# Optimization experiments

Measured on AMD Instinct MI355X. Metric: run time of the kernel, lower is better.

## Reference

```python
import jax, jax.numpy as jnp
import numpy as np

B, C, O, H, W, K, KS = 32, 128, 128, 56, 56, 4, 3
EPS = 1e-5


def setup_inputs() -> dict:
    key = jax.random.key(0)
    ks = jax.random.split(key, 6)
    sc = lambda k, shape, s: jax.random.normal(k, shape, jnp.float32) * s
    return {
        "x": jax.random.normal(ks[0], (B, C, H, W), jnp.float32),
        "fc1_w": sc(ks[1], (K, C), 0.05),
        "fc1_b": jnp.zeros((K,), jnp.float32),
        "fc2_w": sc(ks[2], (K, K), 0.3),
        "fc2_b": jnp.zeros((K,), jnp.float32),
        "weight": sc(ks[3], (K, O, C, KS, KS), 0.05),  # [K, out, in/groups, kh, kw]
        "bias": sc(ks[4], (K, O), 0.05),
        "gamma": jnp.ones((O,), jnp.float32),
        "beta": jnp.zeros((O,), jnp.float32),
    }


def reference(x, fc1_w, fc1_b, fc2_w, fc2_b, weight, bias, gamma, beta):
    # attention2d: global avg pool -> 1x1 conv (== linear) -> relu -> 1x1 conv -> softmax over K
    pooled = x.mean(axis=(2, 3))                          # [B, C]
    h = jax.nn.relu(pooled @ fc1_w.T + fc1_b)             # [B, K]
    attn = jax.nn.softmax(h @ fc2_w.T + fc2_b, axis=-1)   # [B, K]

    # per-sample aggregated kernel / bias
    agg_w = jnp.einsum('bk,koihw->boihw', attn, weight)   # [B, O, C, KS, KS]
    agg_b = attn @ bias                                    # [B, O]

    # per-sample conv (== groups=batch trick in torch)
    def conv_one(xi, wi):
        return jax.lax.conv_general_dilated(
            xi[None], wi, window_strides=(1, 1),
            padding=((1, 1), (1, 1)),
            dimension_numbers=('NCHW', 'OIHW', 'NCHW'))[0]

    out = jax.vmap(conv_one)(x, agg_w) + agg_b[:, :, None, None]  # [B, O, H, W]

    # BatchNorm2d in training mode: biased batch stats over (N, H, W)
    mean = out.mean(axis=(0, 2, 3))
    var = out.var(axis=(0, 2, 3))
    out = (out - mean[None, :, None, None]) * jax.lax.rsqrt(var + EPS)[None, :, None, None]
    out = out * gamma[None, :, None, None] + beta[None, :, None, None]
    return jax.nn.relu(out)
```

## Files before the change

kernel.cpp:

```cpp
#include <hip/hip_runtime.h>
#include <hip/hip_bf16.h>

#define BB 32
#define CC 128
#define OO 128
#define HH 56
#define WW 56
#define KK 4
#define HW 3136
#define WPLANE 147456
#define EPSV 1e-5f

#define NP4 232
#define BUF4 15360

typedef __attribute__((ext_vector_type(8))) short short8v;
typedef __attribute__((ext_vector_type(4))) float f32x4;

static __device__ __forceinline__ void gload16(const void* g, void* l) {
    __builtin_amdgcn_global_load_lds((const __attribute__((address_space(1))) void*)g,
                                     (__attribute__((address_space(3))) void*)l, 16, 0, 0);
}

__global__ void convert_pool_kernel(const float* __restrict__ x,
                                    ushort* __restrict__ xbf,
                                    float* __restrict__ pooledp,
                                    ushort* __restrict__ zpage) {
    const int h = blockIdx.x, b = blockIdx.y;
    if (h == 0 && b == 0 && threadIdx.x < 32) zpage[threadIdx.x] = 0;
    __shared__ float4 xl4[1792];
    const float* xp = x + (size_t)(b * CC) * HW + h * WW;

    #pragma unroll
    for (int k = 0; k < 7; ++k) {
        int u = threadIdx.x + k * 256;
        int c = u / 14, w4 = u - c * 14;
        float4 v = *(const float4*)(xp + (size_t)c * HW + w4 * 4);
        xl4[u ^ ((c >> 3) & 7)] = v;
    }
    __syncthreads();

    const float* xf = (const float*)xl4;
    #pragma unroll
    for (int k = 0; k < 4; ++k) {
        int v = threadIdx.x + k * 256;
        if (v < 896) {
            int w = v >> 4, c8 = v & 15;
            int w4 = w >> 2, wo = w & 3;
            short8v res;
            #pragma unroll
            for (int j = 0; j < 8; ++j) {
                int c = c8 * 8 + j;
                int su = (c * 14 + w4) ^ (c8 & 7);
                __hip_bfloat16 hb = __float2bfloat16(xf[su * 4 + wo]);
                res[j] = *(short*)&hb;
            }
            *(short8v*)(xbf + ((size_t)((b * HH + h) * WW + w)) * CC + c8 * 8) = res;
        }
    }

    if (threadIdx.x < 128) {
        int c = threadIdx.x;
        float s = 0.f;
        #pragma unroll
        for (int w4 = 0; w4 < 14; ++w4) {
            float4 v = xl4[(c * 14 + w4) ^ ((c >> 3) & 7)];
            s += v.x + v.y + v.z + v.w;
        }
        pooledp[((size_t)(b * HH + h)) * CC + c] = s;
    }
}

__global__ void attn_kernel(const float* __restrict__ pooledp,
                            const float* __restrict__ fc1_w, const float* __restrict__ fc1_b,
                            const float* __restrict__ fc2_w, const float* __restrict__ fc2_b,
                            float* __restrict__ attn) {
    const int b = blockIdx.x, c = threadIdx.x;
    float s = 0.f;
    for (int h = 0; h < HH; ++h) s += pooledp[((size_t)(b * HH + h)) * CC + c];
    const float pc = s * (1.0f / HW);
    __shared__ float red[8];
    const int lane = c & 63, wid = c >> 6;
    #pragma unroll
    for (int k = 0; k < KK; ++k) {
        float v = pc * fc1_w[k * CC + c];
        for (int off = 32; off > 0; off >>= 1) v += __shfl_down(v, off, 64);
        if (lane == 0) red[k * 2 + wid] = v;
    }
    __syncthreads();
    if (c == 0) {
        float hk[KK], z[KK], m = -1e30f, den = 0.f;
        #pragma unroll
        for (int k = 0; k < KK; ++k)
            hk[k] = fmaxf(red[k * 2] + red[k * 2 + 1] + fc1_b[k], 0.f);
        #pragma unroll
        for (int k = 0; k < KK; ++k) {
            float t = fc2_b[k];
            #pragma unroll
            for (int j = 0; j < KK; ++j) t += hk[j] * fc2_w[k * KK + j];
            z[k] = t; m = fmaxf(m, t);
        }
        #pragma unroll
        for (int k = 0; k < KK; ++k) { z[k] = expf(z[k] - m); den += z[k]; }
        #pragma unroll
        for (int k = 0; k < KK; ++k) attn[b * KK + k] = z[k] / den;
    }
}

__global__ void aggw_kernel(const float* __restrict__ attn, const float* __restrict__ weight,
                            const float* __restrict__ bias,
                            ushort* __restrict__ aggw, float* __restrict__ agg_b) {
    int idx = blockIdx.x * 256 + threadIdx.x;
    if (idx < BB * 9 * OO * CC) {
        int cc = idx & 31;
        int t1 = idx >> 5;
        int o  = t1 & 127;
        int t2 = t1 >> 7;
        int ci = t2 & 3;
        int t3 = t2 >> 2;
        int j  = t3 % 9;
        int b  = t3 / 9;
        int c  = ci * 32 + cc;
        size_t wi = ((size_t)(o * CC + c)) * 9 + j;
        float s = attn[b*KK + 0] * weight[wi]
                + attn[b*KK + 1] * weight[wi + (size_t)WPLANE]
                + attn[b*KK + 2] * weight[wi + (size_t)2*WPLANE]
                + attn[b*KK + 3] * weight[wi + (size_t)3*WPLANE];
        __hip_bfloat16 hb = __float2bfloat16(s);
        aggw[idx] = *(ushort*)&hb;
    }
    if (blockIdx.x < 16) {
        int i = blockIdx.x * 256 + threadIdx.x;
        int b = i >> 7, o = i & 127;
        float s = 0.f;
        #pragma unroll
        for (int k = 0; k < KK; ++k) s += attn[b*KK + k] * bias[k*OO + o];
        agg_b[i] = s;
    }
}

__launch_bounds__(256, 2)
__global__ void conv_kernel(const ushort* __restrict__ xbf, const ushort* __restrict__ aggw,
                            const float* __restrict__ agg_b, const ushort* __restrict__ zpage,
                            float* __restrict__ out,
                            float* __restrict__ psum, float* __restrict__ psumsq) {
    const int lid  = blockIdx.x;
    const int gwid = (lid & 7) * 112 + (lid >> 3);
    const int b = gwid / 28;
    const int t = gwid - b * 28;
    const int h0 = t * 2;
    __shared__ ushort xs[2 * BUF4 / 2];

    const int tid  = threadIdx.x;
    const int lane = tid & 63;
    const int wid  = tid >> 6;
    const int cf = lane & 15;
    const int kg = lane >> 4;

    const ushort* gp[4]; int gstep[4];
    #pragma unroll
    for (int k = 0; k < 4; ++k) {
        int q = wid + 4 * k;
        int un = q * 64 + lane;
        int u = un ^ ((un >> 3) & 7);
        int pos = u >> 2, quad = u & 3;
        int row = pos / 58, col = pos - row * 58;
        int gh = h0 - 1 + row, gw = col - 1;
        bool valid = (pos < NP4) && (gh >= 0) && (gh < HH) && (gw >= 0) && (gw < WW);
        gp[k] = valid ? (xbf + ((size_t)((b * HH + gh) * WW + gw)) * CC + quad * 8) : zpage;
        gstep[k] = valid ? 32 : 0;
    }

    int blin[7];
    #pragma unroll
    for (int nf = 0; nf < 7; ++nf) {
        int p = nf * 16 + cf;
        int r = p / 56, w = p - r * 56;
        blin[nf] = (((r + 1) * 58 + (w + 1)) << 6) + kg * 16;
    }

    f32x4 acc[2][7];
    #pragma unroll
    for (int mf = 0; mf < 2; ++mf)
        #pragma unroll
        for (int nf = 0; nf < 7; ++nf) acc[mf][nf] = (f32x4){0.f, 0.f, 0.f, 0.f};

    const ushort* Ab = aggw + ((size_t)b * 36) * 4096 + (size_t)(wid * 32 + cf) * 32 + kg * 8;
    #define ALOAD(mf_, j_, ci_) (*(const short8v*)(Ab + (size_t)((j_) * 4 + (ci_)) * 4096 + (mf_) * 512))

    short8v pa[2];
    pa[0] = ALOAD(0, 0, 0);
    pa[1] = ALOAD(1, 0, 0);

    #pragma unroll
    for (int k = 0; k < 4; ++k) {
        int q = wid + 4 * k;
        if (q < 15) { gload16(gp[k], (char*)xs + q * 1024); gp[k] += gstep[k]; }
    }
    __syncthreads();

    int cur = 0;
    for (int ci = 0; ci < 4; ++ci) {
        const char* xbuf = (const char*)xs + cur * BUF4;
        #pragma unroll
        for (int j = 0; j < 9; ++j) {
            const int toff = ((j/3 - 1) * 58 + (j%3 - 1)) * 64;
            short8v ca0 = pa[0], ca1 = pa[1];
            if (j < 8) {
                pa[0] = ALOAD(0, j + 1, ci);
                pa[1] = ALOAD(1, j + 1, ci);
            } else if (ci < 3) {
                pa[0] = ALOAD(0, 0, ci + 1);
                pa[1] = ALOAD(1, 0, ci + 1);
            }
            #pragma unroll
            for (int nf = 0; nf < 7; ++nf) {
                int lin = blin[nf] + toff;
                int swz = lin ^ ((lin >> 3) & 0x70);
                short8v bf = *(const short8v*)(xbuf + swz);
                acc[0][nf] = __builtin_amdgcn_mfma_f32_16x16x32_bf16(ca0, bf, acc[0][nf], 0, 0, 0);
                acc[1][nf] = __builtin_amdgcn_mfma_f32_16x16x32_bf16(ca1, bf, acc[1][nf], 0, 0, 0);
            }
        }
        if (ci < 3) {
            char* base = (char*)xs + (cur ^ 1) * BUF4;
            #pragma unroll
            for (int k = 0; k < 4; ++k) {
                int q = wid + 4 * k;
                if (q < 15) { gload16(gp[k], base + q * 1024); gp[k] += gstep[k]; }
            }
            __syncthreads();
            cur ^= 1;
        }
    }

    #pragma unroll
    for (int mf = 0; mf < 2; ++mf) {
        #pragma unroll
        for (int i = 0; i < 4; ++i) {
            const int o = wid * 32 + mf * 16 + kg * 4 + i;
            const float ab = agg_b[b * OO + o];
            float* op = out + ((size_t)(b * OO + o)) * HW;
            float s = 0.f, s2 = 0.f;
            #pragma unroll
            for (int nf = 0; nf < 7; ++nf) {
                int p = nf * 16 + cf;
                int r = p / 56, w = p - r * 56;
                float v = acc[mf][nf][i] + ab;
                op[(h0 + r) * WW + w] = v;
                s += v; s2 += v * v;
            }
            s  += __shfl_xor(s, 1, 64);  s  += __shfl_xor(s, 2, 64);
            s  += __shfl_xor(s, 4, 64);  s  += __shfl_xor(s, 8, 64);
            s2 += __shfl_xor(s2, 1, 64); s2 += __shfl_xor(s2, 2, 64);
            s2 += __shfl_xor(s2, 4, 64); s2 += __shfl_xor(s2, 8, 64);
            if (cf == 0) {
                psum[gwid * OO + o]   = s;
                psumsq[gwid * OO + o] = s2;
            }
        }
    }
}

__global__ void finstats_kernel(const float* __restrict__ psum, const float* __restrict__ psumsq,
                                float* __restrict__ sums, float* __restrict__ sumsq) {
    const int o = blockIdx.x, l = threadIdx.x;
    float s = 0.f, s2 = 0.f;
    for (int r = l; r < 896; r += 64) { s += psum[r * OO + o]; s2 += psumsq[r * OO + o]; }
    for (int off = 32; off > 0; off >>= 1) {
        s  += __shfl_down(s, off, 64);
        s2 += __shfl_down(s2, off, 64);
    }
    if (l == 0) { sums[o] = s; sumsq[o] = s2; }
}

__global__ void bn_kernel(float* __restrict__ out,
                          const float* __restrict__ sums, const float* __restrict__ sumsq,
                          const float* __restrict__ gamma, const float* __restrict__ beta) {
    const float invN = 1.0f / (float)(BB * HW);
    const int total4 = BB * OO * HW / 4;
    for (int i = blockIdx.x * blockDim.x + threadIdx.x; i < total4; i += gridDim.x * blockDim.x) {
        int o = (i / (HW/4)) % OO;
        float mean = sums[o] * invN;
        float var  = sumsq[o] * invN - mean*mean;
        float inv  = rsqrtf(var + EPSV);
        float g  = gamma[o] * inv;
        float bt = beta[o] - mean * g;
        float4 v = ((float4*)out)[i];
        v.x = fmaxf(v.x*g + bt, 0.f);
        v.y = fmaxf(v.y*g + bt, 0.f);
        v.z = fmaxf(v.z*g + bt, 0.f);
        v.w = fmaxf(v.w*g + bt, 0.f);
        ((float4*)out)[i] = v;
    }
}

extern "C" void kernel_launch(void* const* d_in, const int* in_sizes, int n_in,
                              void* d_out, int out_size, void* d_ws, size_t ws_size,
                              hipStream_t stream) {
    const float* x      = (const float*)d_in[0];
    const float* fc1_w  = (const float*)d_in[1];
    const float* fc1_b  = (const float*)d_in[2];
    const float* fc2_w  = (const float*)d_in[3];
    const float* fc2_b  = (const float*)d_in[4];
    const float* weight = (const float*)d_in[5];
    const float* bias   = (const float*)d_in[6];
    const float* gamma  = (const float*)d_in[7];
    const float* beta   = (const float*)d_in[8];
    float* out = (float*)d_out;

    const size_t XBF_ELEMS  = (size_t)BB * HW * CC;
    const size_t AGGW_ELEMS = (size_t)BB * 9 * OO * CC;
    ushort* xbf  = (ushort*)d_ws;
    ushort* aggw = xbf + XBF_ELEMS;
    float*  wsf  = (float*)(aggw + AGGW_ELEMS);
    float* pooledp = wsf;
    float* attn    = pooledp + 229376;
    float* agg_b   = attn + 128;
    float* psum    = agg_b + 4096;
    float* psumsq  = psum + 114688;
    float* sums    = psumsq + 114688;
    float* sumsq   = sums + 128;
    ushort* zpage  = (ushort*)(sumsq + 128);

    convert_pool_kernel<<<dim3(HH, BB), 256, 0, stream>>>(x, xbf, pooledp, zpage);
    attn_kernel<<<BB, 128, 0, stream>>>(pooledp, fc1_w, fc1_b, fc2_w, fc2_b, attn);
    aggw_kernel<<<(int)((AGGW_ELEMS + 255)/256), 256, 0, stream>>>(attn, weight, bias, aggw, agg_b);
    conv_kernel<<<dim3(896), 256, 0, stream>>>(xbf, aggw, agg_b, zpage, out, psum, psumsq);
    finstats_kernel<<<OO, 64, 0, stream>>>(psum, psumsq, sums, sumsq);
    bn_kernel<<<2048, 256, 0, stream>>>(out, sums, sumsq, gamma, beta);
}
```

Baseline: 110.8 us.

## Use two waves per conv block with 64 output channels each and prefetch B fragments

```diff
diff --git a/kernel.cpp b/kernel.cpp
--- a/kernel.cpp
+++ b/kernel.cpp
@@ -12,7 +12,7 @@
 #define EPSV 1e-5f
 
 #define NP4 232
-#define BUF4 15360
+#define BUF4 16384
 
 typedef __attribute__((ext_vector_type(8))) short short8v;
 typedef __attribute__((ext_vector_type(4))) float f32x4;
@@ -139,7 +139,7 @@
     }
 }
 
-__launch_bounds__(256, 2)
+__launch_bounds__(128, 2)
 __global__ void conv_kernel(const ushort* __restrict__ xbf, const ushort* __restrict__ aggw,
                             const float* __restrict__ agg_b, const ushort* __restrict__ zpage,
                             float* __restrict__ out,
@@ -153,15 +153,15 @@
 
     const int tid  = threadIdx.x;
     const int lane = tid & 63;
-    const int wid  = tid >> 6;
+    const int wg   = tid >> 6;
+
     const int cf = lane & 15;
     const int kg = lane >> 4;
 
-    const ushort* gp[4]; int gstep[4];
-    #pragma unroll
-    for (int k = 0; k < 4; ++k) {
-        int q = wid + 4 * k;
-        int un = q * 64 + lane;
+    const ushort* gp[8]; int gstep[8];
+    #pragma unroll
+    for (int k = 0; k < 8; ++k) {
+        int un = tid + k * 128;
         int u = un ^ ((un >> 3) & 7);
         int pos = u >> 2, quad = u & 3;
         int row = pos / 58, col = pos - row * 58;
@@ -179,66 +179,84 @@
         blin[nf] = (((r + 1) * 58 + (w + 1)) << 6) + kg * 16;
     }
 
-    f32x4 acc[2][7];
-    #pragma unroll
-    for (int mf = 0; mf < 2; ++mf)
+    f32x4 acc[4][7];
+    #pragma unroll
+    for (int mf = 0; mf < 4; ++mf)
         #pragma unroll
         for (int nf = 0; nf < 7; ++nf) acc[mf][nf] = (f32x4){0.f, 0.f, 0.f, 0.f};
 
-    const ushort* Ab = aggw + ((size_t)b * 36) * 4096 + (size_t)(wid * 32 + cf) * 32 + kg * 8;
+    const ushort* Ab = aggw + ((size_t)b * 36) * 4096 + (size_t)(wg * 64 + cf) * 32 + kg * 8;
     #define ALOAD(mf_, j_, ci_) (*(const short8v*)(Ab + (size_t)((j_) * 4 + (ci_)) * 4096 + (mf_) * 512))
 
-    short8v pa[2];
-    pa[0] = ALOAD(0, 0, 0);
-    pa[1] = ALOAD(1, 0, 0);
-
-    #pragma unroll
-    for (int k = 0; k < 4; ++k) {
-        int q = wid + 4 * k;
-        if (q < 15) { gload16(gp[k], (char*)xs + q * 1024); gp[k] += gstep[k]; }
+    short8v pa[4];
+    #pragma unroll
+    for (int mf = 0; mf < 4; ++mf) pa[mf] = ALOAD(mf, 0, 0);
+
+    #pragma unroll
+    for (int k = 0; k < 8; ++k) {
+        gload16(gp[k], (char*)xs + (tid - lane + k * 128) * 16);
+        gp[k] += gstep[k];
     }
     __syncthreads();
 
     int cur = 0;
     for (int ci = 0; ci < 4; ++ci) {
         const char* xbuf = (const char*)xs + cur * BUF4;
+
+        short8v bfc[7], bfn[7];
+        #pragma unroll
+        for (int nf = 0; nf < 7; ++nf) {
+            int lin = blin[nf] + (-58 - 1) * 64;
+            int swz = lin ^ ((lin >> 3) & 0x70);
+            bfc[nf] = *(const short8v*)(xbuf + swz);
+        }
         #pragma unroll
         for (int j = 0; j < 9; ++j) {
-            const int toff = ((j/3 - 1) * 58 + (j%3 - 1)) * 64;
-            short8v ca0 = pa[0], ca1 = pa[1];
             if (j < 8) {
-                pa[0] = ALOAD(0, j + 1, ci);
-                pa[1] = ALOAD(1, j + 1, ci);
+                const int toff = (((j+1)/3 - 1) * 58 + ((j+1)%3 - 1)) * 64;
+                #pragma unroll
+                for (int nf = 0; nf < 7; ++nf) {
+                    int lin = blin[nf] + toff;
+                    int swz = lin ^ ((lin >> 3) & 0x70);
+                    bfn[nf] = *(const short8v*)(xbuf + swz);
+                }
+            }
+            short8v ca[4];
+            #pragma unroll
+            for (int mf = 0; mf < 4; ++mf) ca[mf] = pa[mf];
+            if (j < 8) {
+                #pragma unroll
+                for (int mf = 0; mf < 4; ++mf) pa[mf] = ALOAD(mf, j + 1, ci);
             } else if (ci < 3) {
-                pa[0] = ALOAD(0, 0, ci + 1);
-                pa[1] = ALOAD(1, 0, ci + 1);
+                #pragma unroll
+                for (int mf = 0; mf < 4; ++mf) pa[mf] = ALOAD(mf, 0, ci + 1);
+                char* base = (char*)xs + (cur ^ 1) * BUF4;
+                #pragma unroll
+                for (int k = 0; k < 8; ++k) {
+                    gload16(gp[k], base + (tid - lane + k * 128) * 16);
+                    gp[k] += gstep[k];
+                }
             }
             #pragma unroll
             for (int nf = 0; nf < 7; ++nf) {
-                int lin = blin[nf] + toff;
-                int swz = lin ^ ((lin >> 3) & 0x70);
-                short8v bf = *(const short8v*)(xbuf + swz);
-                acc[0][nf] = __builtin_amdgcn_mfma_f32_16x16x32_bf16(ca0, bf, acc[0][nf], 0, 0, 0);
-                acc[1][nf] = __builtin_amdgcn_mfma_f32_16x16x32_bf16(ca1, bf, acc[1][nf], 0, 0, 0);
-            }
-        }
-        if (ci < 3) {
-            char* base = (char*)xs + (cur ^ 1) * BUF4;
-            #pragma unroll
-            for (int k = 0; k < 4; ++k) {
-                int q = wid + 4 * k;
-                if (q < 15) { gload16(gp[k], base + q * 1024); gp[k] += gstep[k]; }
-            }
-            __syncthreads();
-            cur ^= 1;
-        }
-    }
-
-    #pragma unroll
-    for (int mf = 0; mf < 2; ++mf) {
+                #pragma unroll
+                for (int mf = 0; mf < 4; ++mf)
+                    acc[mf][nf] = __builtin_amdgcn_mfma_f32_16x16x32_bf16(ca[mf], bfc[nf], acc[mf][nf], 0, 0, 0);
+            }
+            if (j < 8) {
+                #pragma unroll
+                for (int nf = 0; nf < 7; ++nf) bfc[nf] = bfn[nf];
+            }
+        }
+        if (ci < 3) __syncthreads();
+        cur ^= 1;
+    }
+
+    #pragma unroll
+    for (int mf = 0; mf < 4; ++mf) {
         #pragma unroll
         for (int i = 0; i < 4; ++i) {
-            const int o = wid * 32 + mf * 16 + kg * 4 + i;
+            const int o = wg * 64 + mf * 16 + kg * 4 + i;
             const float ab = agg_b[b * OO + o];
             float* op = out + ((size_t)(b * OO + o)) * HW;
             float s = 0.f, s2 = 0.f;
@@ -326,7 +344,7 @@
     convert_pool_kernel<<<dim3(HH, BB), 256, 0, stream>>>(x, xbf, pooledp, zpage);
     attn_kernel<<<BB, 128, 0, stream>>>(pooledp, fc1_w, fc1_b, fc2_w, fc2_b, attn);
     aggw_kernel<<<(int)((AGGW_ELEMS + 255)/256), 256, 0, stream>>>(attn, weight, bias, aggw, agg_b);
-    conv_kernel<<<dim3(896), 256, 0, stream>>>(xbf, aggw, agg_b, zpage, out, psum, psumsq);
+    conv_kernel<<<dim3(896), 128, 0, stream>>>(xbf, aggw, agg_b, zpage, out, psum, psumsq);
     finstats_kernel<<<OO, 64, 0, stream>>>(psum, psumsq, sums, sumsq);
     bn_kernel<<<2048, 256, 0, stream>>>(out, sums, sumsq, gamma, beta);
 }
```

Result: no change. 108.8 us (-1.9%).
